# Performance work log

Hardware: AMD Instinct MI355X
Metric: run time of the kernel (lower is better)

Reference implementation:

```python
import jax, jax.numpy as jnp
import numpy as np

# SparseSphereConv (graph_level=6 -> V=40962, kernel_size=9, stride=1, select_index=None)
# Pipeline: neighbor gather -> data-dependent nonzero row selection ->
# per-vertex KxK interpolation matmul -> 1xK conv (linear over C_in,K) -> scatter back.
# With stride=1 / select_index=None the static selection is the identity, so the
# dynamic nonzero selection is equivalent to computing all rows and zeroing the
# rows whose gathered features are entirely zero (selected rows are scattered back,
# unselected rows stay 0 in sparse_reset's zero-initialized output).

BS, C_IN, C_OUT, V, K = 4, 32, 32, 40962, 9

def setup_inputs() -> dict:
    key = jax.random.key(0)
    k1, k2, k3, k4, k5 = jax.random.split(key, 5)
    x = jax.random.normal(k1, (BS, C_IN, V), dtype=jnp.float32)
    index = jax.random.randint(k2, (V, K), 0, V, dtype=jnp.int32)          # neighbor ids per vertex
    itp_mat = jax.random.uniform(k3, (V, K, K), dtype=jnp.float32)         # per-vertex interpolation
    conv_w = jax.random.normal(k4, (C_OUT, C_IN, K), dtype=jnp.float32) * 0.05  # Conv2d(C_in,C_out,(1,K)) weight
    conv_b = jax.random.normal(k5, (C_OUT,), dtype=jnp.float32) * 0.05
    return {"x": x, "index": index, "itp_mat": itp_mat, "conv_w": conv_w, "conv_b": conv_b}

def reference(x, index, itp_mat, conv_w, conv_b):
    # x: [bs, C, V] -> permute(2,0,1) -> gather neighbors -> [V, K, bs, C]
    g = jnp.transpose(x, (2, 0, 1))[index]
    g = jnp.transpose(g, (3, 2, 0, 1))                      # [C, bs, V, K]  (== reshape of [C, bs*V, K])
    # sparse_prepare: keep rows whose min or max over (C, K) is nonzero (detached in torch)
    gd = jax.lax.stop_gradient(g)
    rmin = gd.min(axis=(0, 3))                              # [bs, V]
    rmax = gd.max(axis=(0, 3))                              # [bs, V]
    mask = (rmin != 0) | (rmax != 0)                        # [bs, V]
    # Interploate: [C, S, 1, K] @ [S, K, K] per row -> batched small matmul
    interp = jnp.einsum('cbvk,vkj->cbvj', g, itp_mat)       # [C, bs, V, K]
    # Conv2d with kernel (1, K): contraction over (C_in, K) + bias
    out = jnp.einsum('cbvk,ock->bov', interp, conv_w) + conv_b[None, :, None]  # [bs, C_out, V]
    # sparse_reset: rows not selected stay zero
    return out * mask[:, None, :].astype(out.dtype)
```

## Files before the change

### kernel.cpp

```cpp
#include <hip/hip_runtime.h>

#define NV 40962
#define NK 9
#define CIN 32
#define COUT 32
#define NBS 4
#define VT 256
#define TP 260
#define APAD 296
#define NT 2561
#define PGRID 512
#define NV81 (NV * 81)

typedef __attribute__((ext_vector_type(8))) short bf16x8;
typedef __attribute__((ext_vector_type(4))) float f32x4;

__device__ __forceinline__ unsigned bf16pair(float a, float b) {
    unsigned ua = __float_as_uint(a), ub = __float_as_uint(b);
    ua = (ua + 0x7FFFu + ((ua >> 16) & 1u)) >> 16;
    ub = (ub + 0x7FFFu + ((ub >> 16) & 1u)) & 0xFFFF0000u;
    return (ua & 0xFFFFu) | ub;
}

__device__ __forceinline__ void bar_lgkm() {
    asm volatile("s_waitcnt lgkmcnt(0)\n\ts_barrier" ::: "memory");
}

__global__ void __launch_bounds__(256) transpose_x_bf16(
    const float* __restrict__ x, unsigned* __restrict__ xtw)
{
    __shared__ unsigned T[16 * TP];
    const int b  = blockIdx.x & 3;
    const int v0 = (blockIdx.x >> 2) * VT;
    const int t  = threadIdx.x;
    const int w  = t >> 6;
    const int L  = t & 63;
    const bool full = (v0 + VT <= NV);

    #pragma unroll
    for (int i = 0; i < 4; ++i) {
        const int q = w + 4 * i;
        const float* rowA = x + (size_t)(b * 32 + 2 * q) * NV;
        const float* rowB = rowA + NV;
        #pragma unroll
        for (int h = 0; h < 2; ++h) {
            const int vl = 128 * h + 2 * L;
            float2 a, c;
            if (full) {
                a = *(const float2*)(rowA + v0 + vl);
                c = *(const float2*)(rowB + v0 + vl);
            } else {
                const int v = v0 + vl;
                a.x = (v     < NV) ? rowA[v]     : 0.0f;
                a.y = (v + 1 < NV) ? rowA[v + 1] : 0.0f;
                c.x = (v     < NV) ? rowB[v]     : 0.0f;
                c.y = (v + 1 < NV) ? rowB[v + 1] : 0.0f;
            }
            uint2 d;
            d.x = bf16pair(a.x, c.x);
            d.y = bf16pair(a.y, c.y);
            *(uint2*)&T[q * TP + vl] = d;
        }
    }
    __syncthreads();

    #pragma unroll
    for (int i = 0; i < 4; ++i) {
        const int vl = i * 64 + w * 16 + (L >> 2);
        const int u4 = L & 3;
        const int v  = v0 + vl;
        if (v < NV) {
            uint4 d;
            d.x = T[(4 * u4 + 0) * TP + vl];
            d.y = T[(4 * u4 + 1) * TP + vl];
            d.z = T[(4 * u4 + 2) * TP + vl];
            d.w = T[(4 * u4 + 3) * TP + vl];
            *(uint4*)&xtw[(size_t)v * 64 + b * 16 + 4 * u4] = d;
        }
    }
}

__global__ void __launch_bounds__(256) convert_w_bf16(
    const float* __restrict__ w, unsigned short* __restrict__ wbf)
{
    const int i = blockIdx.x * 256 + threadIdx.x;
    if (i < COUT * CIN * NK) {
        unsigned u = __float_as_uint(w[i]);
        wbf[i] = (unsigned short)((u + 0x7FFFu + ((u >> 16) & 1u)) >> 16);
    }
}

__device__ __forceinline__ void load_itp(float itpv[3],
                                         const float* __restrict__ itp,
                                         int tile, int t)
{
    const size_t base = (size_t)tile * (16 * 81);
    #pragma unroll
    for (int i = 0; i < 3; ++i) {
        const int o = i * 512 + t;
        itpv[i] = (o < 1296 && base + o < (size_t)NV81) ? itp[base + o] : 0.0f;
    }
}

__device__ __forceinline__ void stage_itp(float* __restrict__ buf,
                                          const float itpv[3], int t)
{
    #pragma unroll
    for (int i = 0; i < 3; ++i) {
        const int o = i * 512 + t;
        if (o < 1296) {
            const int vl = o / 81;
            const int r  = o - vl * 81;
            const int kk = r / 9;
            const int jj = r - kk * 9;
            buf[vl * 108 + kk * 12 + jj] = itpv[i];
        }
    }
}

__global__ void __launch_bounds__(512) sparse_conv_mfma(
    const unsigned short* __restrict__ xt, const int* __restrict__ index,
    const float* __restrict__ itp, const unsigned short* __restrict__ wbf,
    const float* __restrict__ bias, float* __restrict__ out)
{
    __shared__ unsigned short Alds[64 * APAD];
    __shared__ float itp_s[2][16 * 108];
    __shared__ unsigned nzv[8][64];

    const int t    = threadIdx.x;
    const int col  = t & 63;
    const int q    = t >> 6;
    const int c0   = q * 4;
    const int b    = col >> 4;
    const int vloc = col & 15;

    int tile = blockIdx.x;
    int idxc[NK];
    {
        const int v = min(tile * 16 + vloc, NV - 1);
        #pragma unroll
        for (int k = 0; k < NK; ++k) idxc[k] = index[v * NK + k];
    }
    float itpv[3];
    load_itp(itpv, itp, tile, t);
    uint2 gath[NK];
    {
        const unsigned short* gb = xt + b * 32 + c0;
        #pragma unroll
        for (int k = 0; k < NK; ++k)
            gath[k] = *(const uint2*)(gb + (size_t)idxc[k] * 128);
    }
    {
        const int tn = min(tile + PGRID, NT - 1);
        const int v  = min(tn * 16 + vloc, NV - 1);
        #pragma unroll
        for (int k = 0; k < NK; ++k) idxc[k] = index[v * NK + k];
    }
    stage_itp(itp_s[0], itpv, t);
    load_itp(itpv, itp, min(tile + PGRID, NT - 1), t);
    bar_lgkm();

    int p = 0;
    for (; tile < NT; tile += PGRID) {
        const int v0 = tile * 16;

        stage_itp(itp_s[p ^ 1], itpv, t);

        const float* ibuf = itp_s[p];
        unsigned nzbits = 0;
        float g[4][NK];
        #pragma unroll
        for (int k = 0; k < NK; ++k) {
            nzbits |= (gath[k].x | gath[k].y) & 0x7FFF7FFFu;
            g[0][k] = __uint_as_float(gath[k].x << 16);
            g[1][k] = __uint_as_float(gath[k].x & 0xFFFF0000u);
            g[2][k] = __uint_as_float(gath[k].y << 16);
            g[3][k] = __uint_as_float(gath[k].y & 0xFFFF0000u);
        }
        float acc[4][NK];
        #pragma unroll
        for (int cc = 0; cc < 4; ++cc)
            #pragma unroll
            for (int j = 0; j < NK; ++j) acc[cc][j] = 0.0f;
        #pragma unroll
        for (int k = 0; k < NK; ++k) {
            const float4 ra = *(const float4*)&ibuf[vloc * 108 + k * 12];
            const float4 rb = *(const float4*)&ibuf[vloc * 108 + k * 12 + 4];
            const float  r8 = ibuf[vloc * 108 + k * 12 + 8];
            const float row[NK] = {ra.x, ra.y, ra.z, ra.w,
                                   rb.x, rb.y, rb.z, rb.w, r8};
            #pragma unroll
            for (int cc = 0; cc < 4; ++cc)
                #pragma unroll
                for (int j = 0; j < NK; ++j)
                    acc[cc][j] += g[cc][k] * row[j];
        }
        {
            unsigned* dst = (unsigned*)&Alds[col * APAD + c0 * 9];
            #pragma unroll
            for (int i = 0; i < 18; ++i) {
                const int f0 = 2 * i, f1 = 2 * i + 1;
                dst[i] = bf16pair(acc[f0 / 9][f0 % 9], acc[f1 / 9][f1 % 9]);
            }
        }
        nzv[q][col] = nzbits;

        {
            const unsigned short* gb = xt + b * 32 + c0;
            #pragma unroll
            for (int k = 0; k < NK; ++k)
                gath[k] = *(const uint2*)(gb + (size_t)idxc[k] * 128);
        }
        {
            const int t2 = min(tile + 2 * PGRID, NT - 1);
            const int v  = min(t2 * 16 + vloc, NV - 1);
            #pragma unroll
            for (int k = 0; k < NK; ++k) idxc[k] = index[v * NK + k];
            load_itp(itpv, itp, t2, t);
        }

        bar_lgkm();

        {
            const int dn = vloc;
            const int dq = col >> 4;
            const int bb = q >> 1;
            const int oh = q & 1;
            const int colw = bb * 16 + dn;

            f32x4 a0 = {0.f, 0.f, 0.f, 0.f};
            #pragma unroll
            for (int ks = 0; ks < 9; ++ks) {
                const int ko = ks * 32 + dq * 8;
                const bf16x8 wa = *(const bf16x8*)(wbf + (oh * 16 + dn) * 288 + ko);
                const bf16x8 bf = *(const bf16x8*)(&Alds[colw * APAD + ko]);
                a0 = __builtin_amdgcn_mfma_f32_16x16x32_bf16(wa, bf, a0, 0, 0, 0);
            }

            const unsigned nz = nzv[0][colw] | nzv[1][colw] |
                                nzv[2][colw] | nzv[3][colw] |
                                nzv[4][colw] | nzv[5][colw] |
                                nzv[6][colw] | nzv[7][colw];
            const float m = nz ? 1.0f : 0.0f;
            const int vv = v0 + dn;
            if (vv < NV) {
                float* outb = out + (size_t)bb * (COUT * NV) + vv;
                #pragma unroll
                for (int r = 0; r < 4; ++r) {
                    const int o = oh * 16 + dq * 4 + r;
                    outb[(size_t)o * NV] = (a0[r] + bias[o]) * m;
                }
            }
        }

        bar_lgkm();
        p ^= 1;
    }
}

extern "C" void kernel_launch(void* const* d_in, const int* in_sizes, int n_in,
                              void* d_out, int out_size, void* d_ws, size_t ws_size,
                              hipStream_t stream)
{
    const float* x     = (const float*)d_in[0];
    const int*   index = (const int*)  d_in[1];
    const float* itp   = (const float*)d_in[2];
    const float* w     = (const float*)d_in[3];
    const float* bias  = (const float*)d_in[4];
    float*       out   = (float*)d_out;

    unsigned short* xt  = (unsigned short*)d_ws;
    unsigned short* wbf = (unsigned short*)((char*)d_ws + (size_t)NV * 128 * 2);

    hipLaunchKernelGGL(convert_w_bf16, dim3((COUT * CIN * NK + 255) / 256),
                       dim3(256), 0, stream, w, wbf);
    const int vtiles = (NV + VT - 1) / VT;
    hipLaunchKernelGGL(transpose_x_bf16, dim3(vtiles * NBS), dim3(256), 0,
                       stream, x, (unsigned*)xt);
    hipLaunchKernelGGL(sparse_conv_mfma, dim3(PGRID), dim3(512), 0,
                       stream, xt, index, itp, wbf, bias, out);
}
```

Before: 145.8 us.

## Fold weight conversion into main kernel, stage indices in LDS, rechunk A layout

```diff
diff --git a/kernel.cpp b/kernel.cpp
--- a/kernel.cpp
+++ b/kernel.cpp
@@ -7,10 +7,10 @@
 #define NBS 4
 #define VT 256
 #define TP 260
-#define APAD 296
 #define NT 2561
 #define PGRID 512
 #define NV81 (NV * 81)
+#define NV9  (NV * 9)
 
 typedef __attribute__((ext_vector_type(8))) short bf16x8;
 typedef __attribute__((ext_vector_type(4))) float f32x4;
@@ -80,21 +80,11 @@
     }
 }
 
-__global__ void __launch_bounds__(256) convert_w_bf16(
-    const float* __restrict__ w, unsigned short* __restrict__ wbf)
-{
-    const int i = blockIdx.x * 256 + threadIdx.x;
-    if (i < COUT * CIN * NK) {
-        unsigned u = __float_as_uint(w[i]);
-        wbf[i] = (unsigned short)((u + 0x7FFFu + ((u >> 16) & 1u)) >> 16);
-    }
-}
-
 __device__ __forceinline__ void load_itp(float itpv[3],
                                          const float* __restrict__ itp,
                                          int tile, int t)
 {
-    const size_t base = (size_t)tile * (16 * 81);
+    const size_t base = (size_t)tile * 1296;
     #pragma unroll
     for (int i = 0; i < 3; ++i) {
         const int o = i * 512 + t;
@@ -118,65 +108,73 @@
     }
 }
 
+__device__ __forceinline__ int load_idx(const int* __restrict__ index,
+                                        int tile, int t)
+{
+    int r = 0;
+    if (t < 144) {
+        const size_t base = (size_t)tile * 144 + t;
+        r = (base < (size_t)NV9) ? index[base] : 0;
+    }
+    return r;
+}
+
 __global__ void __launch_bounds__(512) sparse_conv_mfma(
     const unsigned short* __restrict__ xt, const int* __restrict__ index,
-    const float* __restrict__ itp, const unsigned short* __restrict__ wbf,
+    const float* __restrict__ itp, const float* __restrict__ w,
     const float* __restrict__ bias, float* __restrict__ out)
 {
-    __shared__ unsigned short Alds[64 * APAD];
-    __shared__ float itp_s[2][16 * 108];
+    __shared__ unsigned short Alds[36 * 64 * 8];
+    __shared__ unsigned short Wlds[36 * 32 * 8];
+    __shared__ float itp_s[16 * 108];
+    __shared__ int   idx_s[2][144];
     __shared__ unsigned nzv[8][64];
 
     const int t    = threadIdx.x;
     const int col  = t & 63;
     const int q    = t >> 6;
-    const int c0   = q * 4;
     const int b    = col >> 4;
     const int vloc = col & 15;
+    const unsigned short* gb = xt + b * 32 + q * 4;
 
     int tile = blockIdx.x;
-    int idxc[NK];
+
+    #pragma unroll
+    for (int r = 0; r < 3; ++r) {
+        const int j = t + r * 512;
+        if (j < 1152) {
+            const int o = j & 31;
+            const int c = j >> 5;
+            const float4 f0 = *(const float4*)(w + o * 288 + c * 8);
+            const float4 f1 = *(const float4*)(w + o * 288 + c * 8 + 4);
+            uint4 d;
+            d.x = bf16pair(f0.x, f0.y); d.y = bf16pair(f0.z, f0.w);
+            d.z = bf16pair(f1.x, f1.y); d.w = bf16pair(f1.z, f1.w);
+            *(uint4*)&Wlds[(c * 32 + o) * 8] = d;
+        }
+    }
     {
-        const int v = min(tile * 16 + vloc, NV - 1);
-        #pragma unroll
-        for (int k = 0; k < NK; ++k) idxc[k] = index[v * NK + k];
+        const int i0 = load_idx(index, tile, t);
+        const int i1 = load_idx(index, min(tile + PGRID, NT - 1), t);
+        if (t < 144) { idx_s[0][t] = i0; idx_s[1][t] = i1; }
     }
     float itpv[3];
     load_itp(itpv, itp, tile, t);
+    stage_itp(itp_s, itpv, t);
+    bar_lgkm();
+
     uint2 gath[NK];
-    {
-        const unsigned short* gb = xt + b * 32 + c0;
-        #pragma unroll
-        for (int k = 0; k < NK; ++k)
-            gath[k] = *(const uint2*)(gb + (size_t)idxc[k] * 128);
-    }
-    {
-        const int tn = min(tile + PGRID, NT - 1);
-        const int v  = min(tn * 16 + vloc, NV - 1);
-        #pragma unroll
-        for (int k = 0; k < NK; ++k) idxc[k] = index[v * NK + k];
-    }
-    stage_itp(itp_s[0], itpv, t);
+    #pragma unroll
+    for (int k = 0; k < NK; ++k) {
+        const int nbr = idx_s[0][vloc * 9 + k];
+        gath[k] = *(const uint2*)(gb + (size_t)nbr * 128);
+    }
     load_itp(itpv, itp, min(tile + PGRID, NT - 1), t);
-    bar_lgkm();
-
-    int p = 0;
+    int idxn = load_idx(index, min(tile + 2 * PGRID, NT - 1), t);
+    int cur = 0;
+
     for (; tile < NT; tile += PGRID) {
-        const int v0 = tile * 16;
-
-        stage_itp(itp_s[p ^ 1], itpv, t);
-
-        const float* ibuf = itp_s[p];
         unsigned nzbits = 0;
-        float g[4][NK];
-        #pragma unroll
-        for (int k = 0; k < NK; ++k) {
-            nzbits |= (gath[k].x | gath[k].y) & 0x7FFF7FFFu;
-            g[0][k] = __uint_as_float(gath[k].x << 16);
-            g[1][k] = __uint_as_float(gath[k].x & 0xFFFF0000u);
-            g[2][k] = __uint_as_float(gath[k].y << 16);
-            g[3][k] = __uint_as_float(gath[k].y & 0xFFFF0000u);
-        }
         float acc[4][NK];
         #pragma unroll
         for (int cc = 0; cc < 4; ++cc)
@@ -184,39 +182,43 @@
             for (int j = 0; j < NK; ++j) acc[cc][j] = 0.0f;
         #pragma unroll
         for (int k = 0; k < NK; ++k) {
-            const float4 ra = *(const float4*)&ibuf[vloc * 108 + k * 12];
-            const float4 rb = *(const float4*)&ibuf[vloc * 108 + k * 12 + 4];
-            const float  r8 = ibuf[vloc * 108 + k * 12 + 8];
+            const unsigned lo = gath[k].x, hi = gath[k].y;
+            nzbits |= (lo | hi) & 0x7FFF7FFFu;
+            const float g0 = __uint_as_float(lo << 16);
+            const float g1 = __uint_as_float(lo & 0xFFFF0000u);
+            const float g2 = __uint_as_float(hi << 16);
+            const float g3 = __uint_as_float(hi & 0xFFFF0000u);
+            const float4 ra = *(const float4*)&itp_s[vloc * 108 + k * 12];
+            const float4 rb = *(const float4*)&itp_s[vloc * 108 + k * 12 + 4];
+            const float  r8 = itp_s[vloc * 108 + k * 12 + 8];
             const float row[NK] = {ra.x, ra.y, ra.z, ra.w,
                                    rb.x, rb.y, rb.z, rb.w, r8};
             #pragma unroll
-            for (int cc = 0; cc < 4; ++cc)
-                #pragma unroll
-                for (int j = 0; j < NK; ++j)
-                    acc[cc][j] += g[cc][k] * row[j];
-        }
-        {
-            unsigned* dst = (unsigned*)&Alds[col * APAD + c0 * 9];
-            #pragma unroll
-            for (int i = 0; i < 18; ++i) {
-                const int f0 = 2 * i, f1 = 2 * i + 1;
-                dst[i] = bf16pair(acc[f0 / 9][f0 % 9], acc[f1 / 9][f1 % 9]);
-            }
+            for (int j = 0; j < NK; ++j) {
+                acc[0][j] += g0 * row[j];
+                acc[1][j] += g1 * row[j];
+                acc[2][j] += g2 * row[j];
+                acc[3][j] += g3 * row[j];
+            }
+        }
+        #pragma unroll
+        for (int i2 = 0; i2 < 9; ++i2) {
+            const int k0 = 4 * i2;
+            const int chunk = (9 * q + i2) >> 1;
+            const int off = 4 * ((q + i2) & 1);
+            uint2 d;
+            d.x = bf16pair(acc[k0 / 9][k0 % 9],
+                           acc[(k0 + 1) / 9][(k0 + 1) % 9]);
+            d.y = bf16pair(acc[(k0 + 2) / 9][(k0 + 2) % 9],
+                           acc[(k0 + 3) / 9][(k0 + 3) % 9]);
+            *(uint2*)&Alds[(chunk * 64 + col) * 8 + off] = d;
         }
         nzv[q][col] = nzbits;
 
-        {
-            const unsigned short* gb = xt + b * 32 + c0;
-            #pragma unroll
-            for (int k = 0; k < NK; ++k)
-                gath[k] = *(const uint2*)(gb + (size_t)idxc[k] * 128);
-        }
-        {
-            const int t2 = min(tile + 2 * PGRID, NT - 1);
-            const int v  = min(t2 * 16 + vloc, NV - 1);
-            #pragma unroll
-            for (int k = 0; k < NK; ++k) idxc[k] = index[v * NK + k];
-            load_itp(itpv, itp, t2, t);
+        #pragma unroll
+        for (int k = 0; k < NK; ++k) {
+            const int nbr = idx_s[cur ^ 1][vloc * 9 + k];
+            gath[k] = *(const uint2*)(gb + (size_t)nbr * 128);
         }
 
         bar_lgkm();
@@ -231,9 +233,9 @@
             f32x4 a0 = {0.f, 0.f, 0.f, 0.f};
             #pragma unroll
             for (int ks = 0; ks < 9; ++ks) {
-                const int ko = ks * 32 + dq * 8;
-                const bf16x8 wa = *(const bf16x8*)(wbf + (oh * 16 + dn) * 288 + ko);
-                const bf16x8 bf = *(const bf16x8*)(&Alds[colw * APAD + ko]);
+                const int ch = ks * 4 + dq;
+                const bf16x8 wa = *(const bf16x8*)&Wlds[(ch * 32 + oh * 16 + dn) * 8];
+                const bf16x8 bf = *(const bf16x8*)&Alds[(ch * 64 + colw) * 8];
                 a0 = __builtin_amdgcn_mfma_f32_16x16x32_bf16(wa, bf, a0, 0, 0, 0);
             }
 
@@ -242,7 +244,7 @@
                                 nzv[4][colw] | nzv[5][colw] |
                                 nzv[6][colw] | nzv[7][colw];
             const float m = nz ? 1.0f : 0.0f;
-            const int vv = v0 + dn;
+            const int vv = tile * 16 + dn;
             if (vv < NV) {
                 float* outb = out + (size_t)bb * (COUT * NV) + vv;
                 #pragma unroll
@@ -252,9 +254,13 @@
                 }
             }
         }
+        stage_itp(itp_s, itpv, t);
+        if (t < 144) idx_s[cur][t] = idxn;
+        load_itp(itpv, itp, min(tile + 2 * PGRID, NT - 1), t);
+        idxn = load_idx(index, min(tile + 3 * PGRID, NT - 1), t);
 
         bar_lgkm();
-        p ^= 1;
+        cur ^= 1;
     }
 }
 
@@ -269,14 +275,11 @@
     const float* bias  = (const float*)d_in[4];
     float*       out   = (float*)d_out;
 
-    unsigned short* xt  = (unsigned short*)d_ws;
-    unsigned short* wbf = (unsigned short*)((char*)d_ws + (size_t)NV * 128 * 2);
-
-    hipLaunchKernelGGL(convert_w_bf16, dim3((COUT * CIN * NK + 255) / 256),
-                       dim3(256), 0, stream, w, wbf);
+    unsigned short* xt = (unsigned short*)d_ws;
+
     const int vtiles = (NV + VT - 1) / VT;
     hipLaunchKernelGGL(transpose_x_bf16, dim3(vtiles * NBS), dim3(256), 0,
                        stream, x, (unsigned*)xt);
     hipLaunchKernelGGL(sparse_conv_mfma, dim3(PGRID), dim3(512), 0,
-                       stream, xt, index, itp, wbf, bias, out);
-}
+                       stream, xt, index, itp, w, bias, out);
+}
```

Measured after the change: 139.7 us. 1.04x faster.
